# Optimization experiments

Measured on AMD Instinct MI355X. Metric: run time of the kernel, lower is better.

The kernel has to match this reference:

```python
import jax, jax.numpy as jnp
import numpy as np
from jax import lax

EPS = 1e-5

def _conv1d(x, w, b):
    # x: [B,C,L], w: [O,I,K], valid padding, stride 1
    y = lax.conv_general_dilated(x, w, window_strides=(1,), padding='VALID',
                                 dimension_numbers=('NCH', 'OIH', 'NCH'))
    return y + b[None, :, None]

def setup_inputs() -> dict:
    key = jax.random.key(0)
    ks = jax.random.split(key, 7)
    B, L, C = 16, 4096, 512
    x = jax.random.normal(ks[0], (B, L, C), dtype=jnp.float32)
    fan3 = 1.0 / np.sqrt(C * 3)
    fan1 = 1.0 / np.sqrt(C * 1)
    w_down = jax.random.uniform(ks[1], (C, C, 3), jnp.float32, -fan3, fan3)
    b_down = jax.random.uniform(ks[2], (C,), jnp.float32, -fan3, fan3)
    w_pad = jax.random.uniform(ks[3], (C, C, 1), jnp.float32, -fan1, fan1)
    b_pad = jax.random.uniform(ks[4], (C,), jnp.float32, -fan1, fan1)
    gamma = jnp.ones((C,), jnp.float32)
    beta = jnp.zeros((C,), jnp.float32)
    return {"x": x, "w_down": w_down, "b_down": b_down,
            "w_pad": w_pad, "b_pad": b_pad, "gamma": gamma, "beta": beta}

def reference(x, w_down, b_down, w_pad, b_pad, gamma, beta):
    # d == 2 branch of ConvLayer
    B, L, C = x.shape

    def branch(xs):  # xs: [B, L//2, C]
        xt = jnp.transpose(xs, (0, 2, 1))                 # [B,C,L/2]
        p1 = _conv1d(xt, w_down, b_down)                  # [B,C,L/2-2]
        p2 = _conv1d(xt[:, :, :2], w_pad, b_pad)          # [B,C,2]
        return jnp.concatenate([p1, p2], axis=2)          # [B,C,L/2]

    x1_p = branch(x[:, 0::2, :])
    x2_p = branch(x[:, 1::2, :])
    # interleave: even positions from x1_p, odd from x2_p
    x_p = jnp.stack([x1_p, x2_p], axis=3).reshape(B, C, L)

    # BatchNorm1d in training mode: batch stats over (batch, length)
    mean = jnp.mean(x_p, axis=(0, 2), keepdims=True)
    var = jnp.var(x_p, axis=(0, 2), keepdims=True)
    xn = (x_p - mean) * lax.rsqrt(var + EPS)
    xn = xn * gamma[None, :, None] + beta[None, :, None]

    y = jax.nn.elu(xn)                                    # dropout = identity (eval)
    y = y + jnp.transpose(x, (0, 2, 1))                   # residual [B,C,L]

    # MaxPool1d(kernel=3, stride=2, padding=1)
    yp = jnp.pad(y, ((0, 0), (0, 0), (1, 1)), constant_values=-jnp.inf)
    pooled = lax.reduce_window(yp, -jnp.inf, lax.max, (1, 1, 3), (1, 1, 2), 'VALID')
    return jnp.transpose(pooled, (0, 2, 1))               # [B, L//2, C]
```

## Files before the change

### kernel.cpp

```cpp
#include <hip/hip_runtime.h>
#include <hip/hip_bf16.h>
#include <math.h>

typedef __bf16 bf16;
typedef __bf16 bf16x8 __attribute__((ext_vector_type(8)));
typedef float floatx4 __attribute__((ext_vector_type(4)));

#define GAS __attribute__((address_space(1)))
#define LAS __attribute__((address_space(3)))

static constexpr int B_ = 16, L_ = 4096, C_ = 512;
static constexpr int M_ = B_ * L_;
static constexpr int K_ = 3 * C_;

__global__ void cast_x(const float* __restrict__ x, bf16* __restrict__ xb) {
    const size_t i = ((size_t)blockIdx.x * 256 + threadIdx.x) * 8;
    floatx4 a = *(const floatx4*)(x + i);
    floatx4 b = *(const floatx4*)(x + i + 4);
    bf16x8 o;
#pragma unroll
    for (int j = 0; j < 4; ++j) { o[j] = (bf16)a[j]; o[4 + j] = (bf16)b[j]; }
    *(bf16x8*)(xb + i) = o;
}

__global__ void repack_w(const float* __restrict__ wd, bf16* __restrict__ wr) {
    int idx = blockIdx.x * 256 + threadIdx.x;
    int o   = idx / K_;
    int rem = idx - o * K_;
    int kk  = rem >> 9;
    int i   = rem & 511;
    wr[idx] = (bf16)wd[o * K_ + i * 3 + kk];
}

__global__ __launch_bounds__(256) void gemm_conv(
    const bf16* __restrict__ x, const bf16* __restrict__ wr,
    const float* __restrict__ bd, bf16* __restrict__ xp, float* __restrict__ sums)
{
    __shared__ bf16 As[128 * 64];
    __shared__ bf16 Bs[128 * 64];

    const int tid = threadIdx.x;
    const int u   = blockIdx.x;
    const int mb  = (u & 7) + 8 * (u >> 5);
    const int nb  = (u >> 3) & 3;
    const int m0  = mb * 128;
    const int n0  = nb * 128;

    const int wave = tid >> 6;
    const int lane = tid & 63;
    const int wm = wave & 1;
    const int wn = wave >> 1;
    const int tm = lane & 15;
    const int quad = lane >> 4;

    floatx4 acc[4][4];
#pragma unroll
    for (int i = 0; i < 4; ++i)
#pragma unroll
        for (int j = 0; j < 4; ++j) acc[i][j] = floatx4{0.f, 0.f, 0.f, 0.f};

    int srow[4], ssc[4];
#pragma unroll
    for (int j = 0; j < 4; ++j) {
        const int qa = tid + 256 * j;
        srow[j] = qa >> 3;
        ssc[j]  = (qa & 7) ^ (srow[j] & 7);
    }

    for (int kt = 0; kt < 24; ++kt) {
        const int kk = kt >> 3;
        const int i0 = (kt & 7) << 6;
#pragma unroll
        for (int j = 0; j < 4; ++j) {
            int sr = m0 + srow[j] + 2 * kk; if (sr > M_ - 1) sr = M_ - 1;
            const bf16* sa = x + (size_t)sr * C_ + i0 + ssc[j] * 8;
            __builtin_amdgcn_global_load_lds((const GAS void*)sa,
                (LAS void*)(As + (tid + 256 * j) * 8), 16, 0, 0);
            const bf16* sb = wr + (size_t)(n0 + srow[j]) * K_ + kk * C_ + i0 + ssc[j] * 8;
            __builtin_amdgcn_global_load_lds((const GAS void*)sb,
                (LAS void*)(Bs + (tid + 256 * j) * 8), 16, 0, 0);
        }
        __syncthreads();

#pragma unroll
        for (int ksel = 0; ksel < 2; ++ksel) {
            const int scb = ksel * 4 + quad;
            bf16x8 af[4], bfr[4];
#pragma unroll
            for (int mi = 0; mi < 4; ++mi) {
                const int r = wm * 64 + mi * 16 + tm;
                af[mi] = *(const bf16x8*)(As + r * 64 + ((scb ^ (r & 7)) << 3));
            }
#pragma unroll
            for (int ni = 0; ni < 4; ++ni) {
                const int r = wn * 64 + ni * 16 + tm;
                bfr[ni] = *(const bf16x8*)(Bs + r * 64 + ((scb ^ (r & 7)) << 3));
            }
#pragma unroll
            for (int mi = 0; mi < 4; ++mi)
#pragma unroll
                for (int ni = 0; ni < 4; ++ni)
                    acc[mi][ni] = __builtin_amdgcn_mfma_f32_16x16x32_bf16(af[mi], bfr[ni], acc[mi][ni], 0, 0, 0);
        }
        __syncthreads();
    }

    float bias[4];
#pragma unroll
    for (int ni = 0; ni < 4; ++ni) bias[ni] = bd[n0 + wn * 64 + ni * 16 + tm];

    float s[4] = {0.f, 0.f, 0.f, 0.f}, q[4] = {0.f, 0.f, 0.f, 0.f};
#pragma unroll
    for (int mi = 0; mi < 4; ++mi) {
#pragma unroll
        for (int r = 0; r < 4; ++r) {
            const int m = m0 + wm * 64 + mi * 16 + quad * 4 + r;
            const bool valid = (m & (L_ - 1)) < L_ - 4;
            bf16* dst = xp + (size_t)m * C_ + n0 + wn * 64 + tm;
#pragma unroll
            for (int ni = 0; ni < 4; ++ni) {
                const float v = acc[mi][ni][r] + bias[ni];
                dst[ni * 16] = (bf16)v;
                if (valid) { s[ni] += v; q[ni] += v * v; }
            }
        }
    }
#pragma unroll
    for (int ni = 0; ni < 4; ++ni) {
        float sv = s[ni], qv = q[ni];
        sv += __shfl_xor(sv, 16); sv += __shfl_xor(sv, 32);
        qv += __shfl_xor(qv, 16); qv += __shfl_xor(qv, 32);
        if (quad == 0) {
            const int c = n0 + wn * 64 + ni * 16 + tm;
            atomicAdd(&sums[c], sv);
            atomicAdd(&sums[C_ + c], qv);
        }
    }
}

__global__ void fixup(const float* __restrict__ x, const float* __restrict__ wp,
                      const float* __restrict__ bp, bf16* __restrict__ xp,
                      float* __restrict__ sums)
{
    const int b = blockIdx.x >> 2;
    const int j = blockIdx.x & 3;
    __shared__ float xrow[C_];
    for (int i = threadIdx.x; i < C_; i += 256)
        xrow[i] = x[(size_t)(b * L_ + j) * C_ + i];
    __syncthreads();
    for (int c = threadIdx.x; c < C_; c += 256) {
        const float* w = wp + (size_t)c * C_;
        float acc = 0.f;
#pragma unroll 4
        for (int i = 0; i < C_; i += 4) {
            floatx4 wv = *(const floatx4*)(w + i);
#pragma unroll
            for (int u = 0; u < 4; ++u) acc += wv[u] * xrow[i + u];
        }
        const float v = acc + bp[c];
        xp[(size_t)(b * L_ + 4092 + j) * C_ + c] = (bf16)v;
        atomicAdd(&sums[c], v);
        atomicAdd(&sums[C_ + c], v * v);
    }
}

__global__ void finalize_stats(const float* __restrict__ sums, const float* __restrict__ gamma,
                               const float* __restrict__ beta, float* __restrict__ ss) {
    const int c = threadIdx.x;
    const float invn = 1.0f / 65536.0f;
    float mean = sums[c] * invn;
    float var  = sums[C_ + c] * invn - mean * mean;
    float scale = gamma[c] * rsqrtf(var + 1e-5f);
    ss[c] = scale;
    ss[C_ + c] = beta[c] - mean * scale;
}

__global__ void final_pool(const bf16* __restrict__ xp, const bf16* __restrict__ xb,
                           const float* __restrict__ ss, float* __restrict__ out)
{
    const int gid = blockIdx.x * 256 + threadIdx.x;
    const int cg = gid & 63;
    const int t  = (gid >> 6) & 2047;
    const int b  = gid >> 17;
    const int c0 = cg << 3;

    float sc[8], sh[8];
#pragma unroll
    for (int j = 0; j < 8; ++j) { sc[j] = ss[c0 + j]; sh[j] = ss[C_ + c0 + j]; }

    float best[8];
#pragma unroll
    for (int j = 0; j < 8; ++j) best[j] = -INFINITY;

#pragma unroll
    for (int dl = -1; dl <= 1; ++dl) {
        const int l = 2 * t + dl;
        if (l < 0) continue;
        const size_t off = (size_t)(b * L_ + l) * C_ + c0;
        bf16x8 xpv = *(const bf16x8*)(xp + off);
        bf16x8 xv  = *(const bf16x8*)(xb + off);
#pragma unroll
        for (int j = 0; j < 8; ++j) {
            float z = sc[j] * (float)xpv[j] + sh[j];
            float y = (z > 0.f) ? z : (expf(z) - 1.f);
            y += (float)xv[j];
            best[j] = fmaxf(best[j], y);
        }
    }
    floatx4 o0, o1;
#pragma unroll
    for (int j = 0; j < 4; ++j) { o0[j] = best[j]; o1[j] = best[4 + j]; }
    *(floatx4*)(out + (size_t)gid * 8) = o0;
    *(floatx4*)(out + (size_t)gid * 8 + 4) = o1;
}

extern "C" void kernel_launch(void* const* d_in, const int* in_sizes, int n_in,
                              void* d_out, int out_size, void* d_ws, size_t ws_size,
                              hipStream_t stream)
{
    const float* x      = (const float*)d_in[0];
    const float* w_down = (const float*)d_in[1];
    const float* b_down = (const float*)d_in[2];
    const float* w_pad  = (const float*)d_in[3];
    const float* b_pad  = (const float*)d_in[4];
    const float* gamma  = (const float*)d_in[5];
    const float* beta   = (const float*)d_in[6];
    float* out = (float*)d_out;

    char* ws = (char*)d_ws;
    bf16*  xb   = (bf16*)ws;
    bf16*  xp   = (bf16*)(ws + (size_t)M_ * C_ * 2);
    bf16*  wr   = (bf16*)(ws + (size_t)M_ * C_ * 4);
    float* sums = (float*)(ws + (size_t)M_ * C_ * 4 + (size_t)C_ * K_ * 2);
    float* ss   = sums + 2 * C_;

    hipMemsetAsync(sums, 0, 2 * C_ * sizeof(float), stream);
    cast_x<<<dim3(M_ * C_ / (256 * 8)), dim3(256), 0, stream>>>(x, xb);
    repack_w<<<dim3(3072), dim3(256), 0, stream>>>(w_down, wr);
    gemm_conv<<<dim3(2048), dim3(256), 0, stream>>>(xb, wr, b_down, xp, sums);
    fixup<<<dim3(64), dim3(256), 0, stream>>>(x, w_pad, b_pad, xp, sums);
    finalize_stats<<<dim3(1), dim3(512), 0, stream>>>(sums, gamma, beta, ss);
    final_pool<<<dim3(8192), dim3(256), 0, stream>>>(xp, xb, ss, out);
}
```

Before: 431.0 us.

## Enlarge GEMM tile to 256x256, merge prep kernels, fold stats finalize into pool

The conv GEMM moves from 128x128 tiles with 256 threads to 256x256 tiles with 512 threads, so each wave computes a 64x128 sub-tile. This raises operand reuse and cuts the block count from 2048 to 512. The cast and weight-repack kernels are merged into one launch. The BN finalize kernel is removed: every final_pool thread now recomputes scale and shift itself, and expf becomes __expf. The larger tile needs 64KB of LDS and 128 accumulator registers per thread, which limits occupancy, and 512 blocks may fill the GPU's CUs unevenly.

```diff
diff --git a/kernel.cpp b/kernel.cpp
--- a/kernel.cpp
+++ b/kernel.cpp
@@ -13,56 +13,57 @@
 static constexpr int M_ = B_ * L_;
 static constexpr int K_ = 3 * C_;
 
-__global__ void cast_x(const float* __restrict__ x, bf16* __restrict__ xb) {
-    const size_t i = ((size_t)blockIdx.x * 256 + threadIdx.x) * 8;
-    floatx4 a = *(const floatx4*)(x + i);
-    floatx4 b = *(const floatx4*)(x + i + 4);
-    bf16x8 o;
-#pragma unroll
-    for (int j = 0; j < 4; ++j) { o[j] = (bf16)a[j]; o[4 + j] = (bf16)b[j]; }
-    *(bf16x8*)(xb + i) = o;
-}
-
-__global__ void repack_w(const float* __restrict__ wd, bf16* __restrict__ wr) {
-    int idx = blockIdx.x * 256 + threadIdx.x;
-    int o   = idx / K_;
-    int rem = idx - o * K_;
-    int kk  = rem >> 9;
-    int i   = rem & 511;
-    wr[idx] = (bf16)wd[o * K_ + i * 3 + kk];
-}
-
-__global__ __launch_bounds__(256) void gemm_conv(
+__global__ void prep(const float* __restrict__ x, bf16* __restrict__ xb,
+                     const float* __restrict__ wd, bf16* __restrict__ wr) {
+    if (blockIdx.x < 16384) {
+        const size_t i = ((size_t)blockIdx.x * 256 + threadIdx.x) * 8;
+        floatx4 a = *(const floatx4*)(x + i);
+        floatx4 b = *(const floatx4*)(x + i + 4);
+        bf16x8 o;
+#pragma unroll
+        for (int j = 0; j < 4; ++j) { o[j] = (bf16)a[j]; o[4 + j] = (bf16)b[j]; }
+        *(bf16x8*)(xb + i) = o;
+    } else {
+        int idx = (blockIdx.x - 16384) * 256 + threadIdx.x;
+        int o   = idx / K_;
+        int rem = idx - o * K_;
+        int kk  = rem >> 9;
+        int i   = rem & 511;
+        wr[idx] = (bf16)wd[o * K_ + i * 3 + kk];
+    }
+}
+
+__global__ __launch_bounds__(512, 2) void gemm_conv(
     const bf16* __restrict__ x, const bf16* __restrict__ wr,
     const float* __restrict__ bd, bf16* __restrict__ xp, float* __restrict__ sums)
 {
-    __shared__ bf16 As[128 * 64];
-    __shared__ bf16 Bs[128 * 64];
+    __shared__ bf16 As[256 * 64];
+    __shared__ bf16 Bs[256 * 64];
 
     const int tid = threadIdx.x;
     const int u   = blockIdx.x;
-    const int mb  = (u & 7) + 8 * (u >> 5);
-    const int nb  = (u >> 3) & 3;
-    const int m0  = mb * 128;
-    const int n0  = nb * 128;
+    const int mb  = (u & 7) + 8 * (u >> 4);
+    const int nb  = (u >> 3) & 1;
+    const int m0  = mb * 256;
+    const int n0  = nb * 256;
 
     const int wave = tid >> 6;
     const int lane = tid & 63;
-    const int wm = wave & 1;
-    const int wn = wave >> 1;
+    const int wm = wave & 3;
+    const int wn = wave >> 2;
     const int tm = lane & 15;
     const int quad = lane >> 4;
 
-    floatx4 acc[4][4];
+    floatx4 acc[4][8];
 #pragma unroll
     for (int i = 0; i < 4; ++i)
 #pragma unroll
-        for (int j = 0; j < 4; ++j) acc[i][j] = floatx4{0.f, 0.f, 0.f, 0.f};
+        for (int j = 0; j < 8; ++j) acc[i][j] = floatx4{0.f, 0.f, 0.f, 0.f};
 
     int srow[4], ssc[4];
 #pragma unroll
     for (int j = 0; j < 4; ++j) {
-        const int qa = tid + 256 * j;
+        const int qa = tid + 512 * j;
         srow[j] = qa >> 3;
         ssc[j]  = (qa & 7) ^ (srow[j] & 7);
     }
@@ -75,50 +76,50 @@
             int sr = m0 + srow[j] + 2 * kk; if (sr > M_ - 1) sr = M_ - 1;
             const bf16* sa = x + (size_t)sr * C_ + i0 + ssc[j] * 8;
             __builtin_amdgcn_global_load_lds((const GAS void*)sa,
-                (LAS void*)(As + (tid + 256 * j) * 8), 16, 0, 0);
+                (LAS void*)(As + (tid + 512 * j) * 8), 16, 0, 0);
             const bf16* sb = wr + (size_t)(n0 + srow[j]) * K_ + kk * C_ + i0 + ssc[j] * 8;
             __builtin_amdgcn_global_load_lds((const GAS void*)sb,
-                (LAS void*)(Bs + (tid + 256 * j) * 8), 16, 0, 0);
+                (LAS void*)(Bs + (tid + 512 * j) * 8), 16, 0, 0);
         }
         __syncthreads();
 
 #pragma unroll
         for (int ksel = 0; ksel < 2; ++ksel) {
-            const int scb = ksel * 4 + quad;
-            bf16x8 af[4], bfr[4];
+            const int xo = ((ksel * 4 + quad) ^ (tm & 7)) << 3;
+            bf16x8 af[4], bfr[8];
 #pragma unroll
             for (int mi = 0; mi < 4; ++mi) {
                 const int r = wm * 64 + mi * 16 + tm;
-                af[mi] = *(const bf16x8*)(As + r * 64 + ((scb ^ (r & 7)) << 3));
+                af[mi] = *(const bf16x8*)(As + r * 64 + xo);
             }
 #pragma unroll
-            for (int ni = 0; ni < 4; ++ni) {
-                const int r = wn * 64 + ni * 16 + tm;
-                bfr[ni] = *(const bf16x8*)(Bs + r * 64 + ((scb ^ (r & 7)) << 3));
+            for (int ni = 0; ni < 8; ++ni) {
+                const int r = wn * 128 + ni * 16 + tm;
+                bfr[ni] = *(const bf16x8*)(Bs + r * 64 + xo);
             }
 #pragma unroll
             for (int mi = 0; mi < 4; ++mi)
 #pragma unroll
-                for (int ni = 0; ni < 4; ++ni)
+                for (int ni = 0; ni < 8; ++ni)
                     acc[mi][ni] = __builtin_amdgcn_mfma_f32_16x16x32_bf16(af[mi], bfr[ni], acc[mi][ni], 0, 0, 0);
         }
         __syncthreads();
     }
 
-    float bias[4];
-#pragma unroll
-    for (int ni = 0; ni < 4; ++ni) bias[ni] = bd[n0 + wn * 64 + ni * 16 + tm];
-
-    float s[4] = {0.f, 0.f, 0.f, 0.f}, q[4] = {0.f, 0.f, 0.f, 0.f};
+    float bias[8];
+#pragma unroll
+    for (int ni = 0; ni < 8; ++ni) bias[ni] = bd[n0 + wn * 128 + ni * 16 + tm];
+
+    float s[8] = {0,0,0,0,0,0,0,0}, q[8] = {0,0,0,0,0,0,0,0};
 #pragma unroll
     for (int mi = 0; mi < 4; ++mi) {
 #pragma unroll
         for (int r = 0; r < 4; ++r) {
             const int m = m0 + wm * 64 + mi * 16 + quad * 4 + r;
             const bool valid = (m & (L_ - 1)) < L_ - 4;
-            bf16* dst = xp + (size_t)m * C_ + n0 + wn * 64 + tm;
-#pragma unroll
-            for (int ni = 0; ni < 4; ++ni) {
+            bf16* dst = xp + (size_t)m * C_ + n0 + wn * 128 + tm;
+#pragma unroll
+            for (int ni = 0; ni < 8; ++ni) {
                 const float v = acc[mi][ni][r] + bias[ni];
                 dst[ni * 16] = (bf16)v;
                 if (valid) { s[ni] += v; q[ni] += v * v; }
@@ -126,12 +127,12 @@
         }
     }
 #pragma unroll
-    for (int ni = 0; ni < 4; ++ni) {
+    for (int ni = 0; ni < 8; ++ni) {
         float sv = s[ni], qv = q[ni];
         sv += __shfl_xor(sv, 16); sv += __shfl_xor(sv, 32);
         qv += __shfl_xor(qv, 16); qv += __shfl_xor(qv, 32);
         if (quad == 0) {
-            const int c = n0 + wn * 64 + ni * 16 + tm;
+            const int c = n0 + wn * 128 + ni * 16 + tm;
             atomicAdd(&sums[c], sv);
             atomicAdd(&sums[C_ + c], qv);
         }
@@ -164,19 +165,9 @@
     }
 }
 
-__global__ void finalize_stats(const float* __restrict__ sums, const float* __restrict__ gamma,
-                               const float* __restrict__ beta, float* __restrict__ ss) {
-    const int c = threadIdx.x;
-    const float invn = 1.0f / 65536.0f;
-    float mean = sums[c] * invn;
-    float var  = sums[C_ + c] * invn - mean * mean;
-    float scale = gamma[c] * rsqrtf(var + 1e-5f);
-    ss[c] = scale;
-    ss[C_ + c] = beta[c] - mean * scale;
-}
-
 __global__ void final_pool(const bf16* __restrict__ xp, const bf16* __restrict__ xb,
-                           const float* __restrict__ ss, float* __restrict__ out)
+                           const float* __restrict__ sums, const float* __restrict__ gamma,
+                           const float* __restrict__ beta, float* __restrict__ out)
 {
     const int gid = blockIdx.x * 256 + threadIdx.x;
     const int cg = gid & 63;
@@ -185,8 +176,16 @@
     const int c0 = cg << 3;
 
     float sc[8], sh[8];
-#pragma unroll
-    for (int j = 0; j < 8; ++j) { sc[j] = ss[c0 + j]; sh[j] = ss[C_ + c0 + j]; }
+    const float invn = 1.0f / 65536.0f;
+#pragma unroll
+    for (int j = 0; j < 8; ++j) {
+        const int c = c0 + j;
+        float mean = sums[c] * invn;
+        float var  = sums[C_ + c] * invn - mean * mean;
+        float scale = gamma[c] * rsqrtf(var + 1e-5f);
+        sc[j] = scale;
+        sh[j] = beta[c] - mean * scale;
+    }
 
     float best[8];
 #pragma unroll
@@ -202,7 +201,7 @@
 #pragma unroll
         for (int j = 0; j < 8; ++j) {
             float z = sc[j] * (float)xpv[j] + sh[j];
-            float y = (z > 0.f) ? z : (expf(z) - 1.f);
+            float y = (z > 0.f) ? z : (__expf(z) - 1.f);
             y += (float)xv[j];
             best[j] = fmaxf(best[j], y);
         }
@@ -232,13 +231,10 @@
     bf16*  xp   = (bf16*)(ws + (size_t)M_ * C_ * 2);
     bf16*  wr   = (bf16*)(ws + (size_t)M_ * C_ * 4);
     float* sums = (float*)(ws + (size_t)M_ * C_ * 4 + (size_t)C_ * K_ * 2);
-    float* ss   = sums + 2 * C_;
 
     hipMemsetAsync(sums, 0, 2 * C_ * sizeof(float), stream);
-    cast_x<<<dim3(M_ * C_ / (256 * 8)), dim3(256), 0, stream>>>(x, xb);
-    repack_w<<<dim3(3072), dim3(256), 0, stream>>>(w_down, wr);
-    gemm_conv<<<dim3(2048), dim3(256), 0, stream>>>(xb, wr, b_down, xp, sums);
+    prep<<<dim3(16384 + 3072), dim3(256), 0, stream>>>(x, xb, w_down, wr);
+    gemm_conv<<<dim3(512), dim3(512), 0, stream>>>(xb, wr, b_down, xp, sums);
     fixup<<<dim3(64), dim3(256), 0, stream>>>(x, w_pad, b_pad, xp, sums);
-    finalize_stats<<<dim3(1), dim3(512), 0, stream>>>(sums, gamma, beta, ss);
-    final_pool<<<dim3(8192), dim3(256), 0, stream>>>(xp, xb, ss, out);
-}
+    final_pool<<<dim3(8192), dim3(256), 0, stream>>>(xp, xb, sums, gamma, beta, out);
+}
```

After: 416.8 us. 1.03x faster.
